# Kernel tuning notes

Measured on AMD Instinct MI355X. Metric: run time of the kernel, lower is better.

Reference implementation:

```python
import jax, jax.numpy as jnp
import numpy as np

N, E = 50000, 1600000
IN_DIM, HID, HEADS, DH, NCLS = 1280, 256, 4, 64, 6
NEG_SLOPE = 0.2
LN_EPS = 1e-5


def setup_inputs() -> dict:
    key = jax.random.key(0)
    ks = jax.random.split(key, 24)
    p = {}
    p['x'] = jax.random.normal(ks[0], (N, IN_DIM), dtype=jnp.float32)
    p['edge_index'] = jax.random.randint(ks[1], (2, E), 0, N, dtype=jnp.int64)
    s = 0.05
    p['W_in'] = jax.random.normal(ks[2], (IN_DIM, HID), dtype=jnp.float32) * s
    p['b_in'] = jnp.zeros((HID,), jnp.float32)
    for l in range(2):
        p[f'W_gat{l}'] = jax.random.normal(ks[3 + 6 * l], (HID, HEADS * DH), dtype=jnp.float32) * s
        p[f'att_src{l}'] = jax.random.normal(ks[4 + 6 * l], (HEADS, DH), dtype=jnp.float32) * s
        p[f'att_dst{l}'] = jax.random.normal(ks[5 + 6 * l], (HEADS, DH), dtype=jnp.float32) * s
        p[f'b_gat{l}'] = jnp.zeros((HEADS * DH,), jnp.float32)
        p[f'ln_g{l}'] = jnp.ones((HID,), jnp.float32)
        p[f'ln_b{l}'] = jnp.zeros((HID,), jnp.float32)
    p['W_c1'] = jax.random.normal(ks[20], (HID, HID // 2), dtype=jnp.float32) * s
    p['b_c1'] = jnp.zeros((HID // 2,), jnp.float32)
    p['W_c2'] = jax.random.normal(ks[21], (HID // 2, NCLS), dtype=jnp.float32) * s
    p['b_c2'] = jnp.zeros((NCLS,), jnp.float32)
    return p


def _layer_norm(h, g, b):
    mu = jnp.mean(h, axis=-1, keepdims=True)
    var = jnp.mean((h - mu) ** 2, axis=-1, keepdims=True)
    return (h - mu) * jax.lax.rsqrt(var + LN_EPS) * g + b


def _gat_conv(h, src, dst, W, a_src, a_dst, bias):
    # h: [N, HID] -> per-head projections [N, H, DH]
    xh = (h @ W).reshape(N, HEADS, DH)
    al_src = jnp.sum(xh * a_src, axis=-1)  # [N, H]
    al_dst = jnp.sum(xh * a_dst, axis=-1)  # [N, H]
    e = jax.nn.leaky_relu(al_src[src] + al_dst[dst], NEG_SLOPE)  # [E', H]
    # edge softmax over incoming edges of each destination node
    m = jax.ops.segment_max(e, dst, num_segments=N)
    e = jnp.exp(e - m[dst])
    denom = jax.ops.segment_sum(e, dst, num_segments=N)
    w = e / denom[dst]  # [E', H]
    msg = xh[src] * w[:, :, None]  # [E', H, DH]
    out = jax.ops.segment_sum(msg, dst, num_segments=N)  # [N, H, DH]
    return out.reshape(N, HEADS * DH) + bias


def reference(x, edge_index, W_in, b_in, W_gat0, att_src0, att_dst0, b_gat0, ln_g0, ln_b0,
              W_gat1, att_src1, att_dst1, b_gat1, ln_g1, ln_b1, W_c1, b_c1, W_c2, b_c2):
    # add self loops (PyG GATConv default)
    loop = jnp.arange(N, dtype=edge_index.dtype)
    src = jnp.concatenate([edge_index[0], loop])
    dst = jnp.concatenate([edge_index[1], loop])

    h = jax.nn.relu(x @ W_in + b_in)

    for (Wg, asrc, adst, bg, g, b) in ((W_gat0, att_src0, att_dst0, b_gat0, ln_g0, ln_b0),
                                       (W_gat1, att_src1, att_dst1, b_gat1, ln_g1, ln_b1)):
        h_new = _gat_conv(h, src, dst, Wg, asrc, adst, bg)
        h_new = jax.nn.relu(_layer_norm(h_new, g, b))
        h = h + h_new

    logits = jax.nn.relu(h @ W_c1 + b_c1) @ W_c2 + b_c2
    return logits
```

## Files before the change

### kernel.cpp

```cpp
#include <hip/hip_runtime.h>

#define NN 50000
#define EE 1600000
#define INDIM 1280
#define HID 256
#define HEADS 4
#define DHD 64
#define NCLS 6
#define NEG 0.2f
#define LNEPS 1e-5f

typedef __attribute__((ext_vector_type(8))) short short8;
typedef __attribute__((ext_vector_type(4))) float floatx4;

__device__ __forceinline__ unsigned short f2b(float f) {
    unsigned int u = __float_as_uint(f);
    u += 0x7FFF + ((u >> 16) & 1);
    return (unsigned short)(u >> 16);
}
__device__ __forceinline__ float b2f(unsigned short b) {
    return __uint_as_float(((unsigned int)b) << 16);
}

__global__ void init_cnt_kernel(int* __restrict__ cnt) {
    int n = blockIdx.x * 256 + threadIdx.x;
    if (n < NN) cnt[n] = 1;
}

__global__ void count_edges_kernel(const int* __restrict__ dst, int* __restrict__ cnt) {
    int e = blockIdx.x * 256 + threadIdx.x;
    if (e < EE) atomicAdd(&cnt[dst[e]], 1);
}

__global__ __launch_bounds__(1024) void scan1_kernel(const int* __restrict__ cnt,
                                                     int* __restrict__ scanned,
                                                     int* __restrict__ chtot, int n) {
    __shared__ int wsum[16];
    int tid = threadIdx.x, lane = tid & 63, wv = tid >> 6;
    int i = blockIdx.x * 1024 + tid;
    int s = (i < n) ? cnt[i] : 0;
#pragma unroll
    for (int off = 1; off < 64; off <<= 1) {
        int t = __shfl_up(s, off, 64);
        if (lane >= off) s += t;
    }
    if (lane == 63) wsum[wv] = s;
    __syncthreads();
    if (tid < 16) {
        int ws = wsum[tid];
#pragma unroll
        for (int off = 1; off < 16; off <<= 1) {
            int t = __shfl_up(ws, off, 16);
            if (tid >= off) ws += t;
        }
        wsum[tid] = ws;
    }
    __syncthreads();
    s += (wv > 0) ? wsum[wv - 1] : 0;
    if (i < n) scanned[i] = s;
    if (tid == 1023) chtot[blockIdx.x] = s;
}

__global__ void scan2_kernel(int* __restrict__ chtot, int nch) {
    int lane = threadIdx.x;
    int v = (lane < nch) ? chtot[lane] : 0;
#pragma unroll
    for (int off = 1; off < 64; off <<= 1) {
        int t = __shfl_up(v, off, 64);
        if (lane >= off) v += t;
    }
    if (lane < nch) chtot[lane] = v;
}

__global__ void scan3_kernel(const int* __restrict__ scanned, const int* __restrict__ chtot,
                             int* __restrict__ rowptr, int n) {
    int i = blockIdx.x * 256 + threadIdx.x;
    if (i == 0) rowptr[0] = 0;
    if (i < n) {
        int ch = i >> 10;
        rowptr[i + 1] = scanned[i] + (ch ? chtot[ch - 1] : 0);
    }
}

__global__ void copyfill_kernel(const int* __restrict__ rowptr, int* __restrict__ cursor,
                                int* __restrict__ csr) {
    int n = blockIdx.x * 256 + threadIdx.x;
    if (n < NN) {
        int p = rowptr[n];
        csr[p] = n;
        cursor[n] = p + 1;
    }
}

__global__ void scatter_edges_kernel(const int* __restrict__ src, const int* __restrict__ dst,
                                     int* __restrict__ cursor, int* __restrict__ csr) {
    int e = blockIdx.x * 256 + threadIdx.x;
    if (e < EE) {
        int d = dst[e];
        int pos = atomicAdd(&cursor[d], 1);
        csr[pos] = src[e];
    }
}

__global__ void pack_w_kernel(const float* __restrict__ W, unsigned short* __restrict__ out,
                              int K, int N) {
    int idx = blockIdx.x * 256 + threadIdx.x;
    int total = (K >> 6) * (N >> 4) * 2 * 64;
    if (idx >= total) return;
    int ln = idx & 63;
    int t = idx >> 6;
    int ks = t & 1; t >>= 1;
    int NT = N >> 4;
    int nt = t % NT, kc = t / NT;
    int n = nt * 16 + (ln & 15);
    int k = kc * 64 + ks * 32 + ((ln >> 4) << 3);
    unsigned short u[8];
#pragma unroll
    for (int j = 0; j < 8; j++) u[j] = f2b(W[(size_t)(k + j) * N + n]);
    *(int4*)&out[(size_t)idx * 8] = *(const int4*)u;
}

template <int AF32, int NT, int ACT, int WF32, int WB16>
__global__ __launch_bounds__(256) void fgemm_kernel(const float* __restrict__ Af,
                                                    const unsigned short* __restrict__ Ab,
                                                    const unsigned short* __restrict__ Bf,
                                                    const float* __restrict__ bias,
                                                    float* __restrict__ Cf,
                                                    unsigned short* __restrict__ Cb,
                                                    int M, int K) {
    constexpr int NW = NT / 4;
    int wv = threadIdx.x >> 6, ln = threadIdx.x & 63;
    int m0 = blockIdx.x * 64;
    int kcol = (ln >> 4) << 3;

    size_t arow[4];
#pragma unroll
    for (int mt = 0; mt < 4; mt++) {
        int r = m0 + mt * 16 + (ln & 15);
        arow[mt] = (size_t)min(r, M - 1) * K;
    }

    floatx4 acc[4][NW] = {};

    for (int k0 = 0; k0 < K; k0 += 64) {
#pragma unroll
        for (int ks = 0; ks < 2; ks++) {
            int kb = k0 + ks * 32 + kcol;
            short8 a[4];
#pragma unroll
            for (int mt = 0; mt < 4; mt++) {
                if (AF32) {
                    const float* s = Af + arow[mt] + kb;
                    float4 f0 = *(const float4*)s;
                    float4 f1 = *(const float4*)(s + 4);
                    unsigned short u[8] = {f2b(f0.x), f2b(f0.y), f2b(f0.z), f2b(f0.w),
                                           f2b(f1.x), f2b(f1.y), f2b(f1.z), f2b(f1.w)};
                    a[mt] = *(const short8*)u;
                } else {
                    a[mt] = *(const short8*)(Ab + arow[mt] + kb);
                }
            }
            short8 b[NW];
#pragma unroll
            for (int nw = 0; nw < NW; nw++) {
                size_t boff = ((((size_t)(k0 >> 6) * NT + (wv * NW + nw)) * 2 + ks) * 64 + ln) * 8;
                b[nw] = *(const short8*)(Bf + boff);
            }
#pragma unroll
            for (int nw = 0; nw < NW; nw++)
#pragma unroll
                for (int mt = 0; mt < 4; mt++)
                    acc[mt][nw] = __builtin_amdgcn_mfma_f32_16x16x32_bf16(a[mt], b[nw], acc[mt][nw], 0, 0, 0);
        }
    }

    const int Nout = NT * 16;
#pragma unroll
    for (int mt = 0; mt < 4; mt++) {
#pragma unroll
        for (int nw = 0; nw < NW; nw++) {
            int col = (wv * NW + nw) * 16 + (ln & 15);
            int rb = m0 + mt * 16 + (ln >> 4) * 4;
            float bi = bias ? bias[col] : 0.f;
#pragma unroll
            for (int r = 0; r < 4; r++) {
                int row = rb + r;
                if (row < M) {
                    float v = acc[mt][nw][r] + bi;
                    if (ACT) v = fmaxf(v, 0.f);
                    if (WF32) Cf[(size_t)row * Nout + col] = v;
                    if (WB16) Cb[(size_t)row * Nout + col] = f2b(v);
                }
            }
        }
    }
}

__global__ __launch_bounds__(256) void proj_al_kernel(const unsigned short* __restrict__ xhb,
                                                      const float* __restrict__ a_src,
                                                      const float* __restrict__ a_dst,
                                                      float* __restrict__ al_s,
                                                      float* __restrict__ al_d) {
    int n = blockIdx.x * 4 + (threadIdx.x >> 6);
    if (n >= NN) return;
    int lane = threadIdx.x & 63;
    ushort4 v4 = ((const ushort4*)(xhb + (size_t)n * HID))[lane];
    int base = lane * 4;
    float4 as4 = *(const float4*)&a_src[base];
    float4 ad4 = *(const float4*)&a_dst[base];
    float x0 = b2f(v4.x), x1 = b2f(v4.y), x2 = b2f(v4.z), x3 = b2f(v4.w);
    float ps = x0 * as4.x + x1 * as4.y + x2 * as4.z + x3 * as4.w;
    float pd = x0 * ad4.x + x1 * ad4.y + x2 * ad4.z + x3 * ad4.w;
#pragma unroll
    for (int off = 8; off > 0; off >>= 1) {
        ps += __shfl_down(ps, off, 16);
        pd += __shfl_down(pd, off, 16);
    }
    if ((lane & 15) == 0) {
        int h = lane >> 4;
        al_s[n * 4 + h] = ps;
        al_d[n * 4 + h] = pd;
    }
}

__global__ __launch_bounds__(256) void agg_ln_kernel(const int* __restrict__ rowptr,
                                                     const int* __restrict__ csr,
                                                     const float* __restrict__ al_s,
                                                     const float* __restrict__ al_d,
                                                     const unsigned short* __restrict__ xhb,
                                                     const float* __restrict__ bgat,
                                                     const float* __restrict__ g,
                                                     const float* __restrict__ bb,
                                                     float* __restrict__ h,
                                                     unsigned short* __restrict__ hb) {
    int wv = threadIdx.x >> 6, ln = threadIdx.x & 63;
    int n = blockIdx.x * 4 + wv;
    if (n >= NN) return;
    int start = rowptr[n], end = rowptr[n + 1];
    float4 ad = *(const float4*)&al_d[n * 4];

    float d0 = 0.f, d1 = 0.f, d2 = 0.f, d3 = 0.f;
    for (int i = start + ln; i < end; i += 64) {
        int s = csr[i];
        float4 as = *(const float4*)&al_s[s * 4];
        float e0 = as.x + ad.x; e0 = e0 > 0.f ? e0 : NEG * e0;
        float e1 = as.y + ad.y; e1 = e1 > 0.f ? e1 : NEG * e1;
        float e2 = as.z + ad.z; e2 = e2 > 0.f ? e2 : NEG * e2;
        float e3 = as.w + ad.w; e3 = e3 > 0.f ? e3 : NEG * e3;
        d0 += __expf(e0); d1 += __expf(e1); d2 += __expf(e2); d3 += __expf(e3);
    }
#pragma unroll
    for (int off = 32; off > 0; off >>= 1) {
        d0 += __shfl_xor(d0, off, 64);
        d1 += __shfl_xor(d1, off, 64);
        d2 += __shfl_xor(d2, off, 64);
        d3 += __shfl_xor(d3, off, 64);
    }
    int myh = ln >> 4;
    float invh = 1.f / ((myh == 0) ? d0 : (myh == 1) ? d1 : (myh == 2) ? d2 : d3);
    float adh = (myh == 0) ? ad.x : (myh == 1) ? ad.y : (myh == 2) ? ad.z : ad.w;

    float a0 = 0.f, a1 = 0.f, a2 = 0.f, a3 = 0.f;
#pragma unroll 2
    for (int i = start; i < end; i++) {
        int s = csr[i];
        float e = al_s[s * 4 + myh] + adh;
        e = e > 0.f ? e : NEG * e;
        float w = __expf(e) * invh;
        ushort4 mv = *(const ushort4*)&xhb[(size_t)s * HID + ln * 4];
        a0 = fmaf(w, b2f(mv.x), a0);
        a1 = fmaf(w, b2f(mv.y), a1);
        a2 = fmaf(w, b2f(mv.z), a2);
        a3 = fmaf(w, b2f(mv.w), a3);
    }

    float4 bg = *(const float4*)&bgat[ln * 4];
    float v0 = a0 + bg.x, v1 = a1 + bg.y, v2 = a2 + bg.z, v3 = a3 + bg.w;
    float ps = v0 + v1 + v2 + v3;
    float ps2 = v0 * v0 + v1 * v1 + v2 * v2 + v3 * v3;
#pragma unroll
    for (int off = 32; off > 0; off >>= 1) {
        ps += __shfl_xor(ps, off, 64);
        ps2 += __shfl_xor(ps2, off, 64);
    }
    float mu = ps * (1.f / HID);
    float var = ps2 * (1.f / HID) - mu * mu;
    float rs = rsqrtf(var + LNEPS);
    float4 gg = *(const float4*)&g[ln * 4];
    float4 bbv = *(const float4*)&bb[ln * 4];
    float o0 = fmaxf((v0 - mu) * rs * gg.x + bbv.x, 0.f);
    float o1 = fmaxf((v1 - mu) * rs * gg.y + bbv.y, 0.f);
    float o2 = fmaxf((v2 - mu) * rs * gg.z + bbv.z, 0.f);
    float o3 = fmaxf((v3 - mu) * rs * gg.w + bbv.w, 0.f);
    size_t idx = (size_t)n * HID + ln * 4;
    float4 hv = *(const float4*)&h[idx];
    float4 nh = make_float4(hv.x + o0, hv.y + o1, hv.z + o2, hv.w + o3);
    *(float4*)&h[idx] = nh;
    ushort4 nb = {f2b(nh.x), f2b(nh.y), f2b(nh.z), f2b(nh.w)};
    *(ushort4*)&hb[idx] = nb;
}

__global__ void cls2_kernel(const float* __restrict__ mid, const float* __restrict__ W,
                            const float* __restrict__ bias, float* __restrict__ out) {
    int idx = blockIdx.x * 256 + threadIdx.x;
    if (idx >= NN * NCLS) return;
    int n = idx / NCLS, c = idx % NCLS;
    const float* row = mid + (size_t)n * (HID / 2);
    float acc = bias[c];
#pragma unroll 8
    for (int k = 0; k < HID / 2; k++) acc += row[k] * W[k * NCLS + c];
    out[idx] = acc;
}

extern "C" void kernel_launch(void* const* d_in, const int* in_sizes, int n_in,
                              void* d_out, int out_size, void* d_ws, size_t ws_size,
                              hipStream_t stream) {
    const float* x    = (const float*)d_in[0];
    const int*   ei   = (const int*)d_in[1];
    const float* W_in = (const float*)d_in[2];
    const float* b_in = (const float*)d_in[3];
    const float* W_gat[2]   = {(const float*)d_in[4],  (const float*)d_in[10]};
    const float* att_src[2] = {(const float*)d_in[5],  (const float*)d_in[11]};
    const float* att_dst[2] = {(const float*)d_in[6],  (const float*)d_in[12]};
    const float* b_gat[2]   = {(const float*)d_in[7],  (const float*)d_in[13]};
    const float* ln_g[2]    = {(const float*)d_in[8],  (const float*)d_in[14]};
    const float* ln_b[2]    = {(const float*)d_in[9],  (const float*)d_in[15]};
    const float* W_c1 = (const float*)d_in[16];
    const float* b_c1 = (const float*)d_in[17];
    const float* W_c2 = (const float*)d_in[18];
    const float* b_c2 = (const float*)d_in[19];

    char* ws = (char*)d_ws;
    size_t off = 0;
    auto alloc = [&](size_t bytes) -> void* {
        void* p = ws + off;
        off += (bytes + 255) & ~(size_t)255;
        return p;
    };
    float*          h   = (float*)alloc((size_t)NN * HID * 4);
    unsigned short* hb  = (unsigned short*)alloc((size_t)NN * HID * 2);
    unsigned short* xhb = (unsigned short*)alloc((size_t)NN * HID * 2);
    float* al_s = (float*)alloc((size_t)NN * HEADS * 4);
    float* al_d = (float*)alloc((size_t)NN * HEADS * 4);
    int* rowptr  = (int*)alloc((size_t)(NN + 1) * 4);
    int* cursor  = (int*)alloc((size_t)NN * 4);
    int* csr     = (int*)alloc((size_t)(EE + NN) * 4);
    int* scanned = (int*)alloc((size_t)NN * 4);
    int* chtot   = (int*)alloc(64 * 4);
    unsigned short* WinF = (unsigned short*)alloc((size_t)HID * INDIM * 2);
    unsigned short* WgF0 = (unsigned short*)alloc((size_t)HID * HID * 2);
    unsigned short* WgF1 = (unsigned short*)alloc((size_t)HID * HID * 2);
    unsigned short* Wc1F = (unsigned short*)alloc((size_t)(HID / 2) * HID * 2);
    unsigned short* WgF[2] = {WgF0, WgF1};
    float* mid = (float*)xhb;

    const int* srcv = ei;
    const int* dstv = ei + EE;

    pack_w_kernel<<<(INDIM * HID / 8 + 255) / 256, 256, 0, stream>>>(W_in, WinF, INDIM, HID);
    pack_w_kernel<<<(HID * HID / 8 + 255) / 256, 256, 0, stream>>>(W_gat[0], WgF0, HID, HID);
    pack_w_kernel<<<(HID * HID / 8 + 255) / 256, 256, 0, stream>>>(W_gat[1], WgF1, HID, HID);
    pack_w_kernel<<<(HID * (HID / 2) / 8 + 255) / 256, 256, 0, stream>>>(W_c1, Wc1F, HID, HID / 2);

    int nch = (NN + 1023) / 1024;
    init_cnt_kernel<<<(NN + 255) / 256, 256, 0, stream>>>(cursor);
    count_edges_kernel<<<(EE + 255) / 256, 256, 0, stream>>>(dstv, cursor);
    scan1_kernel<<<nch, 1024, 0, stream>>>(cursor, scanned, chtot, NN);
    scan2_kernel<<<1, 64, 0, stream>>>(chtot, nch);
    scan3_kernel<<<(NN + 255) / 256, 256, 0, stream>>>(scanned, chtot, rowptr, NN);
    copyfill_kernel<<<(NN + 255) / 256, 256, 0, stream>>>(rowptr, cursor, csr);
    scatter_edges_kernel<<<(EE + 255) / 256, 256, 0, stream>>>(srcv, dstv, cursor, csr);

    int MB64 = (NN + 63) / 64;

    fgemm_kernel<1, 16, 1, 1, 1><<<MB64, 256, 0, stream>>>(
        x, nullptr, WinF, b_in, h, hb, NN, INDIM);

    for (int l = 0; l < 2; l++) {
        fgemm_kernel<0, 16, 0, 0, 1><<<MB64, 256, 0, stream>>>(
            nullptr, hb, WgF[l], nullptr, nullptr, xhb, NN, HID);
        proj_al_kernel<<<(NN + 3) / 4, 256, 0, stream>>>(xhb, att_src[l], att_dst[l], al_s, al_d);
        agg_ln_kernel<<<(NN + 3) / 4, 256, 0, stream>>>(rowptr, csr, al_s, al_d, xhb,
                                                        b_gat[l], ln_g[l], ln_b[l], h, hb);
    }

    fgemm_kernel<0, 8, 1, 1, 0><<<MB64, 256, 0, stream>>>(
        nullptr, hb, Wc1F, b_c1, mid, nullptr, NN, HID);
    cls2_kernel<<<(NN * NCLS + 255) / 256, 256, 0, stream>>>(mid, W_c2, b_c2, (float*)d_out);
}
```

Baseline: 1.162 ms.

## Stage A tiles through double-buffered swizzled LDS with register prefetch in GEMMs

Replaces the direct-global-load GEMM with a pipelined version. A tiles are loaded coalesced by all threads, converted to bf16, and written into double-buffered LDS with an XOR swizzle. B fragments and the next A tile are prefetched into registers while MFMAs run on the current tile. The aim is to remove redundant per-wave A reads (each wave previously reloaded the full A tile) and to hide global latency, at the cost of more registers and LDS barriers.

```diff
diff --git a/kernel.cpp b/kernel.cpp
--- a/kernel.cpp
+++ b/kernel.cpp
@@ -21,6 +21,8 @@
 __device__ __forceinline__ float b2f(unsigned short b) {
     return __uint_as_float(((unsigned int)b) << 16);
 }
+
+#define WAIT_LGKM0() __builtin_amdgcn_s_waitcnt(0xC07F)
 
 __global__ void init_cnt_kernel(int* __restrict__ cnt) {
     int n = blockIdx.x * 256 + threadIdx.x;
@@ -120,61 +122,120 @@
     *(int4*)&out[(size_t)idx * 8] = *(const int4*)u;
 }
 
-template <int AF32, int NT, int ACT, int WF32, int WB16>
-__global__ __launch_bounds__(256) void fgemm_kernel(const float* __restrict__ Af,
+template <int AF32, int KI, int NT, int ACT, int WF32, int WB16>
+__global__ __launch_bounds__(256) void pgemm_kernel(const float* __restrict__ Af,
                                                     const unsigned short* __restrict__ Ab,
                                                     const unsigned short* __restrict__ Bf,
                                                     const float* __restrict__ bias,
                                                     float* __restrict__ Cf,
                                                     unsigned short* __restrict__ Cb,
-                                                    int M, int K) {
+                                                    int M) {
     constexpr int NW = NT / 4;
-    int wv = threadIdx.x >> 6, ln = threadIdx.x & 63;
+    constexpr int K = KI * 64;
+    __shared__ __align__(16) unsigned short Als[2][4096];
+    int tid = threadIdx.x, wv = tid >> 6, ln = tid & 63;
     int m0 = blockIdx.x * 64;
-    int kcol = (ln >> 4) << 3;
-
-    size_t arow[4];
-#pragma unroll
-    for (int mt = 0; mt < 4; mt++) {
-        int r = m0 + mt * 16 + (ln & 15);
-        arow[mt] = (size_t)min(r, M - 1) * K;
+
+    int srow[2], scol[2];
+#pragma unroll
+    for (int i = 0; i < 2; i++) {
+        int s = tid + i * 256;
+        int r = s >> 3;
+        srow[i] = min(m0 + r, M - 1);
+        scol[i] = ((s & 7) ^ (r & 7)) * 8;
     }
 
     floatx4 acc[4][NW] = {};
-
-    for (int k0 = 0; k0 < K; k0 += 64) {
+    short8 breg[2][NW * 2];
+    float4 af0[4], af1[4];
+    int4 ai0[2], ai1[2];
+
+    auto issueA = [&](int k, float4* af, int4* ai) {
+#pragma unroll
+        for (int i = 0; i < 2; i++) {
+            if (AF32) {
+                const float* p = Af + (size_t)srow[i] * K + k * 64 + scol[i];
+                af[i * 2] = *(const float4*)p;
+                af[i * 2 + 1] = *(const float4*)(p + 4);
+            } else {
+                ai[i] = *(const int4*)(Ab + (size_t)srow[i] * K + k * 64 + scol[i]);
+            }
+        }
+    };
+    auto issueB = [&](int k, short8* b) {
+#pragma unroll
+        for (int nw = 0; nw < NW; nw++)
+#pragma unroll
+            for (int ks = 0; ks < 2; ks++)
+                b[nw * 2 + ks] = *(const short8*)(
+                    Bf + ((((size_t)k * NT + (wv * NW + nw)) * 2 + ks) * 64 + ln) * 8);
+    };
+    auto writeA = [&](int k, const float4* af, const int4* ai) {
+        unsigned short* dst = &Als[k & 1][0];
+#pragma unroll
+        for (int i = 0; i < 2; i++) {
+            int4 v;
+            if (AF32) {
+                unsigned short u[8] = {f2b(af[2 * i].x), f2b(af[2 * i].y),
+                                       f2b(af[2 * i].z), f2b(af[2 * i].w),
+                                       f2b(af[2 * i + 1].x), f2b(af[2 * i + 1].y),
+                                       f2b(af[2 * i + 1].z), f2b(af[2 * i + 1].w)};
+                v = *(const int4*)u;
+            } else {
+                v = ai[i];
+            }
+            *(int4*)&dst[(tid + i * 256) * 8] = v;
+        }
+    };
+    auto compute = [&](int k, const short8* b) {
+        const unsigned short* src = &Als[k & 1][0];
 #pragma unroll
         for (int ks = 0; ks < 2; ks++) {
-            int kb = k0 + ks * 32 + kcol;
             short8 a[4];
 #pragma unroll
             for (int mt = 0; mt < 4; mt++) {
-                if (AF32) {
-                    const float* s = Af + arow[mt] + kb;
-                    float4 f0 = *(const float4*)s;
-                    float4 f1 = *(const float4*)(s + 4);
-                    unsigned short u[8] = {f2b(f0.x), f2b(f0.y), f2b(f0.z), f2b(f0.w),
-                                           f2b(f1.x), f2b(f1.y), f2b(f1.z), f2b(f1.w)};
-                    a[mt] = *(const short8*)u;
-                } else {
-                    a[mt] = *(const short8*)(Ab + arow[mt] + kb);
-                }
+                int row = mt * 16 + (ln & 15);
+                int g = ks * 4 + (ln >> 4);
+                int off8 = (row >> 3) * 512 + (row & 7) * 64 + (g ^ (row & 7)) * 8;
+                a[mt] = *(const short8*)&src[off8];
             }
-            short8 b[NW];
-#pragma unroll
-            for (int nw = 0; nw < NW; nw++) {
-                size_t boff = ((((size_t)(k0 >> 6) * NT + (wv * NW + nw)) * 2 + ks) * 64 + ln) * 8;
-                b[nw] = *(const short8*)(Bf + boff);
-            }
 #pragma unroll
             for (int nw = 0; nw < NW; nw++)
 #pragma unroll
                 for (int mt = 0; mt < 4; mt++)
-                    acc[mt][nw] = __builtin_amdgcn_mfma_f32_16x16x32_bf16(a[mt], b[nw], acc[mt][nw], 0, 0, 0);
-        }
-    }
-
-    const int Nout = NT * 16;
+                    acc[mt][nw] = __builtin_amdgcn_mfma_f32_16x16x32_bf16(
+                        a[mt], b[nw * 2 + ks], acc[mt][nw], 0, 0, 0);
+        }
+    };
+
+    issueA(0, af0, ai0);
+    issueB(0, breg[0]);
+    writeA(0, af0, ai0);
+    WAIT_LGKM0();
+    __builtin_amdgcn_s_barrier();
+
+#pragma unroll
+    for (int kk = 0; kk < KI / 2; kk++) {
+        int k = kk * 2;
+        issueA(k + 1, af1, ai1);
+        issueB(k + 1, breg[1]);
+        compute(k, breg[0]);
+        writeA(k + 1, af1, ai1);
+        WAIT_LGKM0();
+        __builtin_amdgcn_s_barrier();
+        if (k + 2 < KI) {
+            issueA(k + 2, af0, ai0);
+            issueB(k + 2, breg[0]);
+        }
+        compute(k + 1, breg[1]);
+        if (k + 2 < KI) {
+            writeA(k + 2, af0, ai0);
+            WAIT_LGKM0();
+            __builtin_amdgcn_s_barrier();
+        }
+    }
+
+    constexpr int Nout = NT * 16;
 #pragma unroll
     for (int mt = 0; mt < 4; mt++) {
 #pragma unroll
@@ -373,18 +434,18 @@
 
     int MB64 = (NN + 63) / 64;
 
-    fgemm_kernel<1, 16, 1, 1, 1><<<MB64, 256, 0, stream>>>(
-        x, nullptr, WinF, b_in, h, hb, NN, INDIM);
+    pgemm_kernel<1, 20, 16, 1, 1, 1><<<MB64, 256, 0, stream>>>(
+        x, nullptr, WinF, b_in, h, hb, NN);
 
     for (int l = 0; l < 2; l++) {
-        fgemm_kernel<0, 16, 0, 0, 1><<<MB64, 256, 0, stream>>>(
-            nullptr, hb, WgF[l], nullptr, nullptr, xhb, NN, HID);
+        pgemm_kernel<0, 4, 16, 0, 0, 1><<<MB64, 256, 0, stream>>>(
+            nullptr, hb, WgF[l], nullptr, nullptr, xhb, NN);
         proj_al_kernel<<<(NN + 3) / 4, 256, 0, stream>>>(xhb, att_src[l], att_dst[l], al_s, al_d);
         agg_ln_kernel<<<(NN + 3) / 4, 256, 0, stream>>>(rowptr, csr, al_s, al_d, xhb,
                                                         b_gat[l], ln_g[l], ln_b[l], h, hb);
     }
 
-    fgemm_kernel<0, 8, 1, 1, 0><<<MB64, 256, 0, stream>>>(
-        nullptr, hb, Wc1F, b_c1, mid, nullptr, NN, HID);
+    pgemm_kernel<0, 4, 8, 1, 1, 0><<<MB64, 256, 0, stream>>>(
+        nullptr, hb, Wc1F, b_c1, mid, nullptr, NN);
     cls2_kernel<<<(NN * NCLS + 255) / 256, 256, 0, stream>>>(mid, W_c2, b_c2, (float*)d_out);
 }
```

Result: faster. 1.039 ms (-10.6%).
